# Kernel optimization log

Measured on AMD Instinct MI355X. Metric: run time of the kernel, lower is better.

## Reference

```python
import jax, jax.numpy as jnp
import numpy as np
from jax.scipy.linalg import expm

LATENT, HIDDEN, N_PARTS, K = 128, 2048, 128, 2048
OMEGA_DIM, TRANZ_DIM = 9 * N_PARTS, 3 * N_PARTS


def setup_inputs() -> dict:
    key = jax.random.key(0)
    ks = jax.random.split(key, 10)

    def w(k, out_d, in_d):
        # eqx.nn.Linear-style scale ~ 1/sqrt(fan_in)
        return jax.random.normal(k, (out_d, in_d), dtype=jnp.float32) / np.sqrt(in_d)

    return {
        "x_init": jax.random.normal(ks[0], (LATENT, K), dtype=jnp.float32),
        "Wo0": w(ks[1], HIDDEN, LATENT),
        "Wo1": w(ks[2], HIDDEN, HIDDEN),
        "Wo2": w(ks[3], HIDDEN, HIDDEN),
        "Wo3": w(ks[4], OMEGA_DIM, HIDDEN),
        "Wt0": w(ks[5], HIDDEN, LATENT),
        "Wt1": w(ks[6], HIDDEN, HIDDEN),
        "Wt2": w(ks[7], HIDDEN, HIDDEN),
        "Wt3": w(ks[8], TRANZ_DIM, HIDDEN),
    }


def _mlp(weights, x):
    # bias-free MLP, relu on all but last layer; x is (d_in, K)
    for i, W in enumerate(weights):
        x = W @ x
        if i + 1 < len(weights):
            x = jax.nn.relu(x)
    return x


def reference(x_init, Wo0, Wo1, Wo2, Wo3, Wt0, Wt1, Wt2, Wt3):
    omega = _mlp([Wo0, Wo1, Wo2, Wo3], x_init)            # (9n, K)
    n = omega.shape[0] // 9
    k = omega.shape[1]
    # exp_omega 2D branch: vmap over columns, each column -> (n,3,3) expm batch
    mats = omega.T.reshape(k * n, 3, 3)
    R = jax.vmap(expm)(mats).reshape(k, 9 * n)            # (K, 9n)
    rotations = R.T                                        # (9n, K)
    translations = _mlp([Wt0, Wt1, Wt2, Wt3], x_init)     # (3n, K)
    # form_transformations (2D branch): stack translation as a 4th row -> (12n, K)
    rot_r = rotations.reshape(n, 3, 3, k)
    tr_r = translations.reshape(n, 1, 3, k)
    transf = jnp.concatenate([rot_r, tr_r], axis=1).reshape(-1, k)  # (12n, K)
    return (omega, transf, rotations, translations)
```

## Files before the change

### kernel.cpp

```cpp
#include <hip/hip_runtime.h>
#include <stdint.h>


typedef short bf16x8 __attribute__((ext_vector_type(8)));
typedef float f32x4 __attribute__((ext_vector_type(4)));

__device__ __forceinline__ unsigned short f2bf(float f) {
  unsigned int x = __float_as_uint(f);
  unsigned int r = (x + 0x7fffu + ((x >> 16) & 1u)) >> 16;
  return (unsigned short)r;
}

__device__ __forceinline__ void gld_lds16(const void* g, void* l) {
  __builtin_amdgcn_global_load_lds(
      (__attribute__((address_space(1))) void*)(g),
      (__attribute__((address_space(3))) void*)(l),
      16, 0, 0);
}

__global__ void cast_weights_k(const float* __restrict__ wo0, const float* __restrict__ wo1,
                               const float* __restrict__ wo2, const float* __restrict__ wo3,
                               const float* __restrict__ wt0, const float* __restrict__ wt1,
                               const float* __restrict__ wt2, const float* __restrict__ wt3,
                               unsigned short* __restrict__ dst) {
  int gid = blockIdx.x * 256 + threadIdx.x;
  int idx = gid * 8;
  if (idx >= 20447232) return;
  const float* src;
  int off;
  if (idx < 8650752) {
    if (idx < 262144)       { src = wo0; off = idx; }
    else if (idx < 4456448) { src = wo1; off = idx - 262144; }
    else                    { src = wo2; off = idx - 4456448; }
  } else {
    if (idx < 11010048)      { src = wo3; off = idx - 8650752; }
    else if (idx < 11272192) { src = wt0; off = idx - 11010048; }
    else if (idx < 15466496) { src = wt1; off = idx - 11272192; }
    else if (idx < 19660800) { src = wt2; off = idx - 15466496; }
    else                     { src = wt3; off = idx - 19660800; }
  }
  float4 a = *(const float4*)(src + off);
  float4 b = *(const float4*)(src + off + 4);
  uint4 o;
  o.x = (unsigned)f2bf(a.x) | ((unsigned)f2bf(a.y) << 16);
  o.y = (unsigned)f2bf(a.z) | ((unsigned)f2bf(a.w) << 16);
  o.z = (unsigned)f2bf(b.x) | ((unsigned)f2bf(b.y) << 16);
  o.w = (unsigned)f2bf(b.z) | ((unsigned)f2bf(b.w) << 16);
  *(uint4*)(dst + idx) = o;
}

__global__ void transpose_cast_k(const float* __restrict__ x, unsigned short* __restrict__ xt) {
  __shared__ float tile[32][33];
  const int bx = blockIdx.x, by = blockIdx.y;
  const int tx = threadIdx.x, ty = threadIdx.y;
#pragma unroll
  for (int i = 0; i < 32; i += 8)
    tile[ty + i][tx] = x[(size_t)(by * 32 + ty + i) * 2048 + bx * 32 + tx];
  __syncthreads();
#pragma unroll
  for (int i = 0; i < 32; i += 8)
    xt[(size_t)(bx * 32 + ty + i) * 128 + by * 32 + tx] = f2bf(tile[tx][ty + i]);
}

template <int MODE, int TM, int SWZ>
__global__ __launch_bounds__(256, 2) void gemm_tn(
    const unsigned short* __restrict__ A0, const unsigned short* __restrict__ B0,
    void* __restrict__ C0v, int n0tiles, int ldc0, long csplit0,
    const unsigned short* __restrict__ A1, const unsigned short* __restrict__ B1,
    void* __restrict__ C1v, int ldc1, long csplit1, int Kfull, int Klen) {
  __shared__ alignas(16) unsigned short Asl[TM * 128];
  __shared__ alignas(16) unsigned short Bsl[128 * 128];
  constexpr int TMW = TM / 32;

  int mt, yt;
  if (SWZ) {
    int id = blockIdx.x;
    int xcd = id & 7, s = id >> 3;
    mt = ((xcd & 1) << 3) + (s & 7);
    yt = ((xcd >> 1) << 3) + (s >> 3);
  } else {
    mt = blockIdx.x;
    yt = blockIdx.y;
  }

  const unsigned short* A;
  const unsigned short* B;
  char* C;
  int ldc;
  long csplit;
  if (yt < n0tiles) { A = A0; B = B0; C = (char*)C0v; ldc = ldc0; csplit = csplit0; }
  else { A = A1; B = B1; C = (char*)C1v; ldc = ldc1; csplit = csplit1; yt -= n0tiles; }
  C += (long)blockIdx.z * csplit;

  const int k0base = blockIdx.z * Klen;
  const unsigned short* Ab = A + (size_t)mt * TM * Kfull;
  const unsigned short* Bb = B + (size_t)yt * 128 * Kfull;

  const int tid = threadIdx.x;
  const int wave = tid >> 6, lane = tid & 63;
  const int mw = (wave >> 1) * (TM / 2), nw = (wave & 1) * 64;
  const int l16 = lane & 15, quad = lane >> 4;

  f32x4 acc[TMW][4] = {};

  for (int k0 = k0base; k0 < k0base + Klen; k0 += 128) {
#pragma unroll
    for (int i = 0; i < TM / 16; ++i) {
      int c = i * 256 + tid;
      int row = c >> 4;
      int l = (c & 15) ^ (row & 15);
      gld_lds16(Ab + (size_t)row * Kfull + k0 + l * 8, &Asl[c * 8]);
    }
#pragma unroll
    for (int i = 0; i < 8; ++i) {
      int c = i * 256 + tid;
      int row = c >> 4;
      int l = (c & 15) ^ (row & 15);
      gld_lds16(Bb + (size_t)row * Kfull + k0 + l * 8, &Bsl[c * 8]);
    }
    __syncthreads();

#pragma unroll
    for (int h = 0; h < 4; ++h) {
      bf16x8 af[TMW], bfr[4];
#pragma unroll
      for (int t = 0; t < TMW; ++t) {
        int row = mw + t * 16 + l16;
        int p = (h * 4 + quad) ^ (row & 15);
        af[t] = *(const bf16x8*)&Asl[row * 128 + p * 8];
      }
#pragma unroll
      for (int t = 0; t < 4; ++t) {
        int row = nw + t * 16 + l16;
        int p = (h * 4 + quad) ^ (row & 15);
        bfr[t] = *(const bf16x8*)&Bsl[row * 128 + p * 8];
      }
#pragma unroll
      for (int tm = 0; tm < TMW; ++tm)
#pragma unroll
        for (int tn = 0; tn < 4; ++tn)
          acc[tm][tn] = __builtin_amdgcn_mfma_f32_16x16x32_bf16(af[tm], bfr[tn], acc[tm][tn], 0, 0, 0);
    }
    __syncthreads();
  }

  const int mbase = mt * TM + mw;
  const int nbase = yt * 128 + nw;
#pragma unroll
  for (int tm = 0; tm < TMW; ++tm) {
#pragma unroll
    for (int tn = 0; tn < 4; ++tn) {
      int col = nbase + tn * 16 + l16;
      int row0 = mbase + tm * 16 + quad * 4;
      if (MODE == 0) {
#pragma unroll
        for (int r = 0; r < 4; ++r) {
          float v = fmaxf(acc[tm][tn][r], 0.0f);
          ((unsigned short*)C)[(size_t)(row0 + r) * ldc + col] = f2bf(v);
        }
      } else {
        *(f32x4*)((float*)C + (size_t)col * ldc + row0) = acc[tm][tn];
      }
    }
  }
}

__device__ __forceinline__ void mm3(const float* a, const float* b, float* c) {
#pragma unroll
  for (int r = 0; r < 3; ++r)
#pragma unroll
    for (int cc = 0; cc < 3; ++cc)
      c[r * 3 + cc] = a[r * 3 + 0] * b[0 + cc] + a[r * 3 + 1] * b[3 + cc] + a[r * 3 + 2] * b[6 + cc];
}

__global__ void finalize_k(const float* __restrict__ om_p, const float* __restrict__ tr_p,
                           float* __restrict__ out) {
  const int k = blockIdx.x * 256 + threadIdx.x;
  const int j = blockIdx.y;

  float a[9];
#pragma unroll
  for (int i = 0; i < 9; ++i)
    a[i] = om_p[(size_t)(9 * j + i) * 2048 + k] + om_p[2359296 + (size_t)(9 * j + i) * 2048 + k];

  float* omega  = out;
  float* transf = out + (size_t)1152 * 2048;
  float* rot    = out + (size_t)(1152 + 1536) * 2048;
  float* transl = out + (size_t)(1152 + 1536 + 1152) * 2048;

#pragma unroll
  for (int i = 0; i < 9; ++i) omega[(size_t)(9 * j + i) * 2048 + k] = a[i];

  float n1 = 0.f;
#pragma unroll
  for (int c = 0; c < 3; ++c) {
    float s = fabsf(a[c]) + fabsf(a[3 + c]) + fabsf(a[6 + c]);
    n1 = fmaxf(n1, s);
  }
  int s = 0;
  if (n1 > 0.25f) {
    s = (int)ceilf(log2f(n1 * 4.0f));
    if (s < 0) s = 0;
  }
  const float scl = exp2f((float)(-s));
  float As[9];
#pragma unroll
  for (int i = 0; i < 9; ++i) As[i] = a[i] * scl;

  float E[9] = {1, 0, 0, 0, 1, 0, 0, 0, 1};
  float T[9] = {1, 0, 0, 0, 1, 0, 0, 0, 1};
#pragma unroll
  for (int t = 1; t <= 12; ++t) {
    float Tn[9];
    mm3(T, As, Tn);
    const float inv = 1.0f / (float)t;
#pragma unroll
    for (int i = 0; i < 9; ++i) { T[i] = Tn[i] * inv; E[i] += T[i]; }
  }
  for (int q = 0; q < s; ++q) {
    float Tn[9];
    mm3(E, E, Tn);
#pragma unroll
    for (int i = 0; i < 9; ++i) E[i] = Tn[i];
  }

#pragma unroll
  for (int i = 0; i < 9; ++i) {
    rot[(size_t)(9 * j + i) * 2048 + k] = E[i];
    transf[(size_t)(12 * j + i) * 2048 + k] = E[i];
  }
  float tr[3];
#pragma unroll
  for (int c = 0; c < 3; ++c)
    tr[c] = tr_p[(size_t)(3 * j + c) * 2048 + k] + tr_p[786432 + (size_t)(3 * j + c) * 2048 + k];
#pragma unroll
  for (int c = 0; c < 3; ++c) {
    transf[(size_t)(12 * j + 9 + c) * 2048 + k] = tr[c];
    transl[(size_t)(3 * j + c) * 2048 + k] = tr[c];
  }
}

extern "C" void kernel_launch(void* const* d_in, const int* in_sizes, int n_in,
                              void* d_out, int out_size, void* d_ws, size_t ws_size,
                              hipStream_t stream) {
  const float* x   = (const float*)d_in[0];
  const float* Wo0 = (const float*)d_in[1];
  const float* Wo1 = (const float*)d_in[2];
  const float* Wo2 = (const float*)d_in[3];
  const float* Wo3 = (const float*)d_in[4];
  const float* Wt0 = (const float*)d_in[5];
  const float* Wt1 = (const float*)d_in[6];
  const float* Wt2 = (const float*)d_in[7];
  const float* Wt3 = (const float*)d_in[8];

  unsigned short* wb   = (unsigned short*)d_ws;
  unsigned short* wo0b = wb + 0;
  unsigned short* wo1b = wb + 262144;
  unsigned short* wo2b = wb + 4456448;
  unsigned short* wo3b = wb + 8650752;
  unsigned short* wt0b = wb + 11010048;
  unsigned short* wt1b = wb + 11272192;
  unsigned short* wt2b = wb + 15466496;
  unsigned short* wt3b = wb + 19660800;
  unsigned short* Xt   = wb + 20447232;
  unsigned short* HoA  = Xt + 262144;
  unsigned short* HoB  = HoA + 4194304;
  unsigned short* HtA  = HoB + 4194304;
  unsigned short* HtB  = HtA + 4194304;
  float* om_p = (float*)(HtB + 4194304);
  float* tr_p = om_p + 2 * 2359296;

  cast_weights_k<<<9984, 256, 0, stream>>>(Wo0, Wo1, Wo2, Wo3, Wt0, Wt1, Wt2, Wt3, wb);
  transpose_cast_k<<<dim3(64, 4), dim3(32, 8), 0, stream>>>(x, Xt);

  gemm_tn<0, 128, 1><<<512, 256, 0, stream>>>(Xt, wo0b, HoA, 16, 2048, 0,
                                              Xt, wt0b, HtA, 2048, 0, 128, 128);
  gemm_tn<0, 128, 1><<<512, 256, 0, stream>>>(HoA, wo1b, HoB, 16, 2048, 0,
                                              HtA, wt1b, HtB, 2048, 0, 2048, 2048);
  gemm_tn<0, 128, 1><<<512, 256, 0, stream>>>(HoB, wo2b, HoA, 16, 2048, 0,
                                              HtB, wt2b, HtA, 2048, 0, 2048, 2048);
  gemm_tn<1, 64, 0><<<dim3(32, 12, 2), 256, 0, stream>>>(
      HoA, wo3b, om_p, 9, 2048, (long)2359296 * 4,
      HtA, wt3b, tr_p, 2048, (long)786432 * 4, 2048, 1024);

  finalize_k<<<dim3(8, 128), 256, 0, stream>>>(om_p, tr_p, (float*)d_out);
}
```

Measured before the change: 246.1 us.

## Fuse final-layer GEMM with expm epilogue and merge prep kernels

```diff
diff --git a/kernel.cpp b/kernel.cpp
--- a/kernel.cpp
+++ b/kernel.cpp
@@ -18,13 +18,29 @@
       16, 0, 0);
 }
 
-__global__ void cast_weights_k(const float* __restrict__ wo0, const float* __restrict__ wo1,
-                               const float* __restrict__ wo2, const float* __restrict__ wo3,
-                               const float* __restrict__ wt0, const float* __restrict__ wt1,
-                               const float* __restrict__ wt2, const float* __restrict__ wt3,
-                               unsigned short* __restrict__ dst) {
-  int gid = blockIdx.x * 256 + threadIdx.x;
-  int idx = gid * 8;
+__global__ void prep_k(const float* __restrict__ x,
+                       const float* __restrict__ wo0, const float* __restrict__ wo1,
+                       const float* __restrict__ wo2, const float* __restrict__ wo3,
+                       const float* __restrict__ wt0, const float* __restrict__ wt1,
+                       const float* __restrict__ wt2, const float* __restrict__ wt3,
+                       unsigned short* __restrict__ dst, unsigned short* __restrict__ xt) {
+  __shared__ float tile[32][33];
+  const int b = blockIdx.x;
+  const int tid = threadIdx.x;
+  if (b >= 9984) {
+    const int r = b - 9984;
+    const int bx = r & 63, by = r >> 6;
+    const int tx = tid & 31, ty = tid >> 5;
+#pragma unroll
+    for (int i = 0; i < 32; i += 8)
+      tile[ty + i][tx] = x[(size_t)(by * 32 + ty + i) * 2048 + bx * 32 + tx];
+    __syncthreads();
+#pragma unroll
+    for (int i = 0; i < 32; i += 8)
+      xt[(size_t)(bx * 32 + ty + i) * 128 + by * 32 + tx] = f2bf(tile[tx][ty + i]);
+    return;
+  }
+  int idx = (b * 256 + tid) * 8;
   if (idx >= 20447232) return;
   const float* src;
   int off;
@@ -40,37 +56,23 @@
     else                     { src = wt3; off = idx - 19660800; }
   }
   float4 a = *(const float4*)(src + off);
-  float4 b = *(const float4*)(src + off + 4);
+  float4 c = *(const float4*)(src + off + 4);
   uint4 o;
   o.x = (unsigned)f2bf(a.x) | ((unsigned)f2bf(a.y) << 16);
   o.y = (unsigned)f2bf(a.z) | ((unsigned)f2bf(a.w) << 16);
-  o.z = (unsigned)f2bf(b.x) | ((unsigned)f2bf(b.y) << 16);
-  o.w = (unsigned)f2bf(b.z) | ((unsigned)f2bf(b.w) << 16);
+  o.z = (unsigned)f2bf(c.x) | ((unsigned)f2bf(c.y) << 16);
+  o.w = (unsigned)f2bf(c.z) | ((unsigned)f2bf(c.w) << 16);
   *(uint4*)(dst + idx) = o;
 }
 
-__global__ void transpose_cast_k(const float* __restrict__ x, unsigned short* __restrict__ xt) {
-  __shared__ float tile[32][33];
-  const int bx = blockIdx.x, by = blockIdx.y;
-  const int tx = threadIdx.x, ty = threadIdx.y;
-#pragma unroll
-  for (int i = 0; i < 32; i += 8)
-    tile[ty + i][tx] = x[(size_t)(by * 32 + ty + i) * 2048 + bx * 32 + tx];
-  __syncthreads();
-#pragma unroll
-  for (int i = 0; i < 32; i += 8)
-    xt[(size_t)(bx * 32 + ty + i) * 128 + by * 32 + tx] = f2bf(tile[tx][ty + i]);
-}
-
-template <int MODE, int TM, int SWZ>
+template <int SWZ>
 __global__ __launch_bounds__(256, 2) void gemm_tn(
     const unsigned short* __restrict__ A0, const unsigned short* __restrict__ B0,
-    void* __restrict__ C0v, int n0tiles, int ldc0, long csplit0,
+    unsigned short* __restrict__ C0, int n0tiles, int ldc0,
     const unsigned short* __restrict__ A1, const unsigned short* __restrict__ B1,
-    void* __restrict__ C1v, int ldc1, long csplit1, int Kfull, int Klen) {
-  __shared__ alignas(16) unsigned short Asl[TM * 128];
+    unsigned short* __restrict__ C1, int ldc1, int K) {
+  __shared__ alignas(16) unsigned short Asl[128 * 128];
   __shared__ alignas(16) unsigned short Bsl[128 * 128];
-  constexpr int TMW = TM / 32;
 
   int mt, yt;
   if (SWZ) {
@@ -85,46 +87,37 @@
 
   const unsigned short* A;
   const unsigned short* B;
-  char* C;
+  unsigned short* C;
   int ldc;
-  long csplit;
-  if (yt < n0tiles) { A = A0; B = B0; C = (char*)C0v; ldc = ldc0; csplit = csplit0; }
-  else { A = A1; B = B1; C = (char*)C1v; ldc = ldc1; csplit = csplit1; yt -= n0tiles; }
-  C += (long)blockIdx.z * csplit;
-
-  const int k0base = blockIdx.z * Klen;
-  const unsigned short* Ab = A + (size_t)mt * TM * Kfull;
-  const unsigned short* Bb = B + (size_t)yt * 128 * Kfull;
+  if (yt < n0tiles) { A = A0; B = B0; C = C0; ldc = ldc0; }
+  else { A = A1; B = B1; C = C1; ldc = ldc1; yt -= n0tiles; }
+
+  const unsigned short* Ab = A + (size_t)mt * 128 * K;
+  const unsigned short* Bb = B + (size_t)yt * 128 * K;
 
   const int tid = threadIdx.x;
   const int wave = tid >> 6, lane = tid & 63;
-  const int mw = (wave >> 1) * (TM / 2), nw = (wave & 1) * 64;
+  const int mw = (wave >> 1) * 64, nw = (wave & 1) * 64;
   const int l16 = lane & 15, quad = lane >> 4;
 
-  f32x4 acc[TMW][4] = {};
-
-  for (int k0 = k0base; k0 < k0base + Klen; k0 += 128) {
-#pragma unroll
-    for (int i = 0; i < TM / 16; ++i) {
-      int c = i * 256 + tid;
-      int row = c >> 4;
-      int l = (c & 15) ^ (row & 15);
-      gld_lds16(Ab + (size_t)row * Kfull + k0 + l * 8, &Asl[c * 8]);
-    }
+  f32x4 acc[4][4] = {};
+
+  for (int k0 = 0; k0 < K; k0 += 128) {
 #pragma unroll
     for (int i = 0; i < 8; ++i) {
       int c = i * 256 + tid;
       int row = c >> 4;
       int l = (c & 15) ^ (row & 15);
-      gld_lds16(Bb + (size_t)row * Kfull + k0 + l * 8, &Bsl[c * 8]);
+      gld_lds16(Ab + (size_t)row * K + k0 + l * 8, &Asl[c * 8]);
+      gld_lds16(Bb + (size_t)row * K + k0 + l * 8, &Bsl[c * 8]);
     }
     __syncthreads();
 
 #pragma unroll
     for (int h = 0; h < 4; ++h) {
-      bf16x8 af[TMW], bfr[4];
-#pragma unroll
-      for (int t = 0; t < TMW; ++t) {
+      bf16x8 af[4], bfr[4];
+#pragma unroll
+      for (int t = 0; t < 4; ++t) {
         int row = mw + t * 16 + l16;
         int p = (h * 4 + quad) ^ (row & 15);
         af[t] = *(const bf16x8*)&Asl[row * 128 + p * 8];
@@ -136,7 +129,7 @@
         bfr[t] = *(const bf16x8*)&Bsl[row * 128 + p * 8];
       }
 #pragma unroll
-      for (int tm = 0; tm < TMW; ++tm)
+      for (int tm = 0; tm < 4; ++tm)
 #pragma unroll
         for (int tn = 0; tn < 4; ++tn)
           acc[tm][tn] = __builtin_amdgcn_mfma_f32_16x16x32_bf16(af[tm], bfr[tn], acc[tm][tn], 0, 0, 0);
@@ -144,22 +137,18 @@
     __syncthreads();
   }
 
-  const int mbase = mt * TM + mw;
+  const int mbase = mt * 128 + mw;
   const int nbase = yt * 128 + nw;
 #pragma unroll
-  for (int tm = 0; tm < TMW; ++tm) {
+  for (int tm = 0; tm < 4; ++tm) {
 #pragma unroll
     for (int tn = 0; tn < 4; ++tn) {
       int col = nbase + tn * 16 + l16;
       int row0 = mbase + tm * 16 + quad * 4;
-      if (MODE == 0) {
-#pragma unroll
-        for (int r = 0; r < 4; ++r) {
-          float v = fmaxf(acc[tm][tn][r], 0.0f);
-          ((unsigned short*)C)[(size_t)(row0 + r) * ldc + col] = f2bf(v);
-        }
-      } else {
-        *(f32x4*)((float*)C + (size_t)col * ldc + row0) = acc[tm][tn];
+#pragma unroll
+      for (int r = 0; r < 4; ++r) {
+        float v = fmaxf(acc[tm][tn][r], 0.0f);
+        C[(size_t)(row0 + r) * ldc + col] = f2bf(v);
       }
     }
   }
@@ -173,70 +162,189 @@
       c[r * 3 + cc] = a[r * 3 + 0] * b[0 + cc] + a[r * 3 + 1] * b[3 + cc] + a[r * 3 + 2] * b[6 + cc];
 }
 
-__global__ void finalize_k(const float* __restrict__ om_p, const float* __restrict__ tr_p,
-                           float* __restrict__ out) {
-  const int k = blockIdx.x * 256 + threadIdx.x;
-  const int j = blockIdx.y;
-
-  float a[9];
-#pragma unroll
-  for (int i = 0; i < 9; ++i)
-    a[i] = om_p[(size_t)(9 * j + i) * 2048 + k] + om_p[2359296 + (size_t)(9 * j + i) * 2048 + k];
+__device__ __forceinline__ void expm3(const float* a, float* E) {
+  float n1 = 0.f;
+#pragma unroll
+  for (int c = 0; c < 3; ++c) {
+    float s = fabsf(a[c]) + fabsf(a[3 + c]) + fabsf(a[6 + c]);
+    n1 = fmaxf(n1, s);
+  }
+  int s = 0;
+  if (n1 > 0.25f) {
+    s = (int)ceilf(log2f(n1 * 4.0f));
+    if (s < 0) s = 0;
+  }
+  const float scl = exp2f((float)(-s));
+  float As[9];
+#pragma unroll
+  for (int i = 0; i < 9; ++i) As[i] = a[i] * scl;
+  float T[9] = {1, 0, 0, 0, 1, 0, 0, 0, 1};
+#pragma unroll
+  for (int i = 0; i < 9; ++i) E[i] = T[i];
+#pragma unroll
+  for (int t = 1; t <= 12; ++t) {
+    float Tn[9];
+    mm3(T, As, Tn);
+    const float inv = 1.0f / (float)t;
+#pragma unroll
+    for (int i = 0; i < 9; ++i) { T[i] = Tn[i] * inv; E[i] += T[i]; }
+  }
+  for (int q = 0; q < s; ++q) {
+    float Tn[9];
+    mm3(E, E, Tn);
+#pragma unroll
+    for (int i = 0; i < 9; ++i) E[i] = Tn[i];
+  }
+}
+
+__global__ __launch_bounds__(256, 2) void gemm_l3(
+    const unsigned short* __restrict__ Ho, const unsigned short* __restrict__ W9,
+    const unsigned short* __restrict__ Ht, const unsigned short* __restrict__ W3,
+    float* __restrict__ out) {
+  __shared__ alignas(16) char smem[16384 + 39168];
+  unsigned short* Asl = (unsigned short*)smem;
+  unsigned short* Bsl = (unsigned short*)(smem + 16384);
+  float* Cl = (float*)(smem + 16384);
+
+  const int mt = blockIdx.x;
+  const int yt = blockIdx.y;
+  const int tid = threadIdx.x;
+  const int wave = tid >> 6, lane = tid & 63;
+  const int l16 = lane & 15, quad = lane >> 4;
+  const int mbase = mt * 64;
 
   float* omega  = out;
   float* transf = out + (size_t)1152 * 2048;
   float* rot    = out + (size_t)(1152 + 1536) * 2048;
   float* transl = out + (size_t)(1152 + 1536 + 1152) * 2048;
 
-#pragma unroll
-  for (int i = 0; i < 9; ++i) omega[(size_t)(9 * j + i) * 2048 + k] = a[i];
-
-  float n1 = 0.f;
-#pragma unroll
-  for (int c = 0; c < 3; ++c) {
-    float s = fabsf(a[c]) + fabsf(a[3 + c]) + fabsf(a[6 + c]);
-    n1 = fmaxf(n1, s);
-  }
-  int s = 0;
-  if (n1 > 0.25f) {
-    s = (int)ceilf(log2f(n1 * 4.0f));
-    if (s < 0) s = 0;
-  }
-  const float scl = exp2f((float)(-s));
-  float As[9];
-#pragma unroll
-  for (int i = 0; i < 9; ++i) As[i] = a[i] * scl;
-
-  float E[9] = {1, 0, 0, 0, 1, 0, 0, 0, 1};
-  float T[9] = {1, 0, 0, 0, 1, 0, 0, 0, 1};
-#pragma unroll
-  for (int t = 1; t <= 12; ++t) {
-    float Tn[9];
-    mm3(T, As, Tn);
-    const float inv = 1.0f / (float)t;
-#pragma unroll
-    for (int i = 0; i < 9; ++i) { T[i] = Tn[i] * inv; E[i] += T[i]; }
-  }
-  for (int q = 0; q < s; ++q) {
-    float Tn[9];
-    mm3(E, E, Tn);
-#pragma unroll
-    for (int i = 0; i < 9; ++i) E[i] = Tn[i];
-  }
-
-#pragma unroll
-  for (int i = 0; i < 9; ++i) {
-    rot[(size_t)(9 * j + i) * 2048 + k] = E[i];
-    transf[(size_t)(12 * j + i) * 2048 + k] = E[i];
-  }
-  float tr[3];
-#pragma unroll
-  for (int c = 0; c < 3; ++c)
-    tr[c] = tr_p[(size_t)(3 * j + c) * 2048 + k] + tr_p[786432 + (size_t)(3 * j + c) * 2048 + k];
-#pragma unroll
-  for (int c = 0; c < 3; ++c) {
-    transf[(size_t)(12 * j + 9 + c) * 2048 + k] = tr[c];
-    transl[(size_t)(3 * j + c) * 2048 + k] = tr[c];
+  if (yt < 8) {
+    const unsigned short* Ab = Ho + (size_t)mbase * 2048;
+    const unsigned short* Bb = W9 + (size_t)yt * 144 * 2048;
+    const int mw = wave * 16;
+    f32x4 acc[9] = {};
+
+    for (int k0 = 0; k0 < 2048; k0 += 128) {
+#pragma unroll
+      for (int i = 0; i < 4; ++i) {
+        int c = i * 256 + tid;
+        int row = c >> 4;
+        int l = (c & 15) ^ (row & 15);
+        gld_lds16(Ab + (size_t)row * 2048 + k0 + l * 8, &Asl[c * 8]);
+      }
+#pragma unroll
+      for (int i = 0; i < 9; ++i) {
+        int c = i * 256 + tid;
+        int row = c >> 4;
+        int l = (c & 15) ^ (row & 15);
+        gld_lds16(Bb + (size_t)row * 2048 + k0 + l * 8, &Bsl[c * 8]);
+      }
+      __syncthreads();
+#pragma unroll
+      for (int h = 0; h < 4; ++h) {
+        bf16x8 af;
+        {
+          int row = mw + l16;
+          int p = (h * 4 + quad) ^ (row & 15);
+          af = *(const bf16x8*)&Asl[row * 128 + p * 8];
+        }
+#pragma unroll
+        for (int t = 0; t < 9; ++t) {
+          int row = t * 16 + l16;
+          int p = (h * 4 + quad) ^ (row & 15);
+          bf16x8 bf = *(const bf16x8*)&Bsl[row * 128 + p * 8];
+          acc[t] = __builtin_amdgcn_mfma_f32_16x16x32_bf16(af, bf, acc[t], 0, 0, 0);
+        }
+      }
+      __syncthreads();
+    }
+
+#pragma unroll
+    for (int t = 0; t < 9; ++t) {
+      int d = t * 16 + l16;
+      int s0 = mw + quad * 4;
+      *(f32x4*)&Cl[d * 68 + s0] = acc[t];
+    }
+    __syncthreads();
+
+    const int jbase = yt * 16;
+    const int k = mbase + lane;
+#pragma unroll 1
+    for (int pp = 0; pp < 4; ++pp) {
+      int pl = wave * 4 + pp;
+      int j = jbase + pl;
+      float a[9];
+#pragma unroll
+      for (int i = 0; i < 9; ++i) a[i] = Cl[(pl * 9 + i) * 68 + lane];
+#pragma unroll
+      for (int i = 0; i < 9; ++i) omega[(size_t)(9 * j + i) * 2048 + k] = a[i];
+      float E[9];
+      expm3(a, E);
+#pragma unroll
+      for (int i = 0; i < 9; ++i) {
+        rot[(size_t)(9 * j + i) * 2048 + k] = E[i];
+        transf[(size_t)(12 * j + i) * 2048 + k] = E[i];
+      }
+    }
+  } else {
+    const int nt = yt - 8;
+    const unsigned short* Ab = Ht + (size_t)mbase * 2048;
+    const unsigned short* Bb = W3 + (size_t)nt * 128 * 2048;
+    const int mw = (wave >> 1) * 32, nw = (wave & 1) * 64;
+    f32x4 acc[2][4] = {};
+
+    for (int k0 = 0; k0 < 2048; k0 += 128) {
+#pragma unroll
+      for (int i = 0; i < 4; ++i) {
+        int c = i * 256 + tid;
+        int row = c >> 4;
+        int l = (c & 15) ^ (row & 15);
+        gld_lds16(Ab + (size_t)row * 2048 + k0 + l * 8, &Asl[c * 8]);
+      }
+#pragma unroll
+      for (int i = 0; i < 8; ++i) {
+        int c = i * 256 + tid;
+        int row = c >> 4;
+        int l = (c & 15) ^ (row & 15);
+        gld_lds16(Bb + (size_t)row * 2048 + k0 + l * 8, &Bsl[c * 8]);
+      }
+      __syncthreads();
+#pragma unroll
+      for (int h = 0; h < 4; ++h) {
+        bf16x8 af[2], bfr[4];
+#pragma unroll
+        for (int t = 0; t < 2; ++t) {
+          int row = mw + t * 16 + l16;
+          int p = (h * 4 + quad) ^ (row & 15);
+          af[t] = *(const bf16x8*)&Asl[row * 128 + p * 8];
+        }
+#pragma unroll
+        for (int t = 0; t < 4; ++t) {
+          int row = nw + t * 16 + l16;
+          int p = (h * 4 + quad) ^ (row & 15);
+          bfr[t] = *(const bf16x8*)&Bsl[row * 128 + p * 8];
+        }
+#pragma unroll
+        for (int tm = 0; tm < 2; ++tm)
+#pragma unroll
+          for (int tn = 0; tn < 4; ++tn)
+            acc[tm][tn] = __builtin_amdgcn_mfma_f32_16x16x32_bf16(af[tm], bfr[tn], acc[tm][tn], 0, 0, 0);
+      }
+      __syncthreads();
+    }
+
+    const int nbase = nt * 128 + nw;
+#pragma unroll
+    for (int tm = 0; tm < 2; ++tm) {
+#pragma unroll
+      for (int tn = 0; tn < 4; ++tn) {
+        int n = nbase + tn * 16 + l16;
+        int row0 = mbase + mw + tm * 16 + quad * 4;
+        int j = n / 3, c = n % 3;
+        *(f32x4*)&transl[(size_t)n * 2048 + row0] = acc[tm][tn];
+        *(f32x4*)&transf[(size_t)(12 * j + 9 + c) * 2048 + row0] = acc[tm][tn];
+      }
+    }
   }
 }
 
@@ -267,21 +375,14 @@
   unsigned short* HoB  = HoA + 4194304;
   unsigned short* HtA  = HoB + 4194304;
   unsigned short* HtB  = HtA + 4194304;
-  float* om_p = (float*)(HtB + 4194304);
-  float* tr_p = om_p + 2 * 2359296;
-
-  cast_weights_k<<<9984, 256, 0, stream>>>(Wo0, Wo1, Wo2, Wo3, Wt0, Wt1, Wt2, Wt3, wb);
-  transpose_cast_k<<<dim3(64, 4), dim3(32, 8), 0, stream>>>(x, Xt);
-
-  gemm_tn<0, 128, 1><<<512, 256, 0, stream>>>(Xt, wo0b, HoA, 16, 2048, 0,
-                                              Xt, wt0b, HtA, 2048, 0, 128, 128);
-  gemm_tn<0, 128, 1><<<512, 256, 0, stream>>>(HoA, wo1b, HoB, 16, 2048, 0,
-                                              HtA, wt1b, HtB, 2048, 0, 2048, 2048);
-  gemm_tn<0, 128, 1><<<512, 256, 0, stream>>>(HoB, wo2b, HoA, 16, 2048, 0,
-                                              HtB, wt2b, HtA, 2048, 0, 2048, 2048);
-  gemm_tn<1, 64, 0><<<dim3(32, 12, 2), 256, 0, stream>>>(
-      HoA, wo3b, om_p, 9, 2048, (long)2359296 * 4,
-      HtA, wt3b, tr_p, 2048, (long)786432 * 4, 2048, 1024);
-
-  finalize_k<<<dim3(8, 128), 256, 0, stream>>>(om_p, tr_p, (float*)d_out);
-}
+
+  prep_k<<<10240, 256, 0, stream>>>(x, Wo0, Wo1, Wo2, Wo3, Wt0, Wt1, Wt2, Wt3, wb, Xt);
+
+  gemm_tn<1><<<512, 256, 0, stream>>>(Xt, wo0b, HoA, 16, 2048,
+                                      Xt, wt0b, HtA, 2048, 128);
+  gemm_tn<1><<<512, 256, 0, stream>>>(HoA, wo1b, HoB, 16, 2048,
+                                      HtA, wt1b, HtB, 2048, 2048);
+  gemm_tn<1><<<512, 256, 0, stream>>>(HoB, wo2b, HoA, 16, 2048,
+                                      HtB, wt2b, HtA, 2048, 2048);
+  gemm_l3<<<dim3(32, 11), 256, 0, stream>>>(HoA, wo3b, HtA, wt3b, (float*)d_out);
+}
```

After: 240.5 us. 2.2% less time.
